# Kernel tuning notes

Measured on AMD Instinct MI355X. Metric: run time of the kernel, lower is better.

The kernel has to match this reference:

```python
import jax, jax.numpy as jnp
import numpy as np

BN_EPS = 1e-5


def setup_inputs() -> dict:
    key = jax.random.key(0)
    ks = jax.random.split(key, 5)
    B, N, M, C = 2, 8192, 8192, 3
    return {
        "x": jax.random.normal(ks[0], (B, N, C), dtype=jnp.float32),
        "y": jax.random.normal(ks[1], (B, M, C), dtype=jnp.float32),
        "W1": jax.random.normal(ks[2], (256, 20), dtype=jnp.float32) * 0.1,
        "gamma1": jnp.ones((256,), jnp.float32),
        "beta1": jnp.zeros((256,), jnp.float32),
        "mean1": jnp.zeros((256,), jnp.float32),
        "var1": jnp.ones((256,), jnp.float32),
        "W2": jax.random.normal(ks[3], (128, 256), dtype=jnp.float32) * 0.1,
        "gamma2": jnp.ones((128,), jnp.float32),
        "beta2": jnp.zeros((128,), jnp.float32),
        "mean2": jnp.zeros((128,), jnp.float32),
        "var2": jnp.ones((128,), jnp.float32),
        "W3": jax.random.normal(ks[4], (1, 128), dtype=jnp.float32) * 0.1,
        "k": 20,
    }


def _bn(x, gamma, beta, mean, var):
    # x: [B, C, N]; inference-mode BatchNorm1d
    inv = gamma * jax.lax.rsqrt(var + BN_EPS)
    return x * inv[None, :, None] + (beta - mean * inv)[None, :, None]


def reference(x, y, W1, gamma1, beta1, mean1, var1,
              W2, gamma2, beta2, mean2, var2, W3, k):
    # x: [B,N,C], y: [B,M,C]
    xx = jnp.sum(x * x, axis=-1)                      # [B,N]
    yy = jnp.sum(y * y, axis=-1)                      # [B,M]
    inner = jnp.einsum('bnc,bmc->bnm', x, y)          # [B,N,M]
    # negative squared pairwise distance (as in torch code)
    pd = 2.0 * inner - xx[:, :, None] - yy[:, None, :]
    dist, _ = jax.lax.top_k(pd, k)                    # [B,N,k], descending = k nearest
    feat = jnp.transpose(dist, (0, 2, 1))             # [B,k,N]
    h = jax.nn.relu(_bn(jnp.einsum('oc,bcn->bon', W1, feat), gamma1, beta1, mean1, var1))
    h = jax.nn.relu(_bn(jnp.einsum('oc,bcn->bon', W2, h), gamma2, beta2, mean2, var2))
    out = jax.nn.sigmoid(jnp.einsum('oc,bcn->bon', W3, h))  # [B,1,N]
    return jnp.transpose(out, (0, 2, 1))              # [B,N,1]
```

## Files before the change

### kernel.cpp

```cpp
#include <hip/hip_runtime.h>
#include <hip/hip_bf16.h>
#include <math.h>


#define M_CAND 8192
#define NROWS 16384
#define KSEL 20
#define MPL 4

__device__ __forceinline__ float med3f(float a, float b, float c) {
    return __builtin_amdgcn_fmed3f(a, b, c);
}

__global__ __launch_bounds__(256) void k_prep(const float* __restrict__ y,
                                              const float* __restrict__ w2,
                                              float* __restrict__ ys,
                                              float* __restrict__ w2t) {
    int idx = blockIdx.x * 256 + threadIdx.x;
    if (idx < NROWS) {
        int b = idx >> 13, m = idx & 8191;
        const float* p = y + (size_t)idx * 3;
        float y0 = p[0], y1 = p[1], y2 = p[2];
        float* base = ys + (size_t)b * 4 * M_CAND + m;
        base[0]          = y0;
        base[M_CAND]     = y1;
        base[2 * M_CAND] = y2;
        base[3 * M_CAND] = -(y0 * y0 + y1 * y1 + y2 * y2);
    } else {
        int j = idx - NROWS;
        int o = j >> 8, kk = j & 255;
        w2t[kk * 128 + o] = w2[j];
    }
}

__global__ __launch_bounds__(256, 4) void k_knn(const float* __restrict__ x,
                                                const float* __restrict__ ys,
                                                float* __restrict__ dfeat) {
    __shared__ float sm[4][64 * 21];
    const int wid  = threadIdx.x >> 6;
    const int lane = threadIdx.x & 63;
    const int row  = blockIdx.x * 4 + wid;
    const int b    = row >> 13;
    const float x0 = x[row * 3 + 0];
    const float x1 = x[row * 3 + 1];
    const float x2 = x[row * 3 + 2];
    const float tx0 = 2.0f * x0, tx1 = 2.0f * x1, tx2 = 2.0f * x2;
    const float xxn = -(x0 * x0 + x1 * x1 + x2 * x2);
    const float4* q0 = (const float4*)(ys + (size_t)(b * 4 + 0) * M_CAND) + lane;
    const float4* q1 = (const float4*)(ys + (size_t)(b * 4 + 1) * M_CAND) + lane;
    const float4* q2 = (const float4*)(ys + (size_t)(b * 4 + 2) * M_CAND) + lane;
    const float4* q3 = (const float4*)(ys + (size_t)(b * 4 + 3) * M_CAND) + lane;

    float bl[MPL];
#pragma unroll
    for (int j = 0; j < MPL; ++j) bl[j] = -3.0e38f;

    float4 c0 = q0[0], c1 = q1[0], c2 = q2[0], c3 = q3[0];
#pragma unroll 1
    for (int t = 0; t < 32; ++t) {
        const int nt = ((t + 1) & 31) * 64;
        float4 n0 = q0[nt], n1 = q1[nt], n2 = q2[nt], n3 = q3[nt];
        const float* e0 = (const float*)&c0;
        const float* e1 = (const float*)&c1;
        const float* e2 = (const float*)&c2;
        const float* e3 = (const float*)&c3;
#pragma unroll
        for (int j = 0; j < 4; ++j) {
            float v = fmaf(tx0, e0[j], fmaf(tx1, e1[j], fmaf(tx2, e2[j], xxn))) + e3[j];
            bl[3] = med3f(v, bl[2], bl[3]);
            bl[2] = med3f(v, bl[1], bl[2]);
            bl[1] = med3f(v, bl[0], bl[1]);
            bl[0] = fmaxf(bl[0], v);
        }
        c0 = n0; c1 = n1; c2 = n2; c3 = n3;
    }

    float* myp = sm[wid] + lane * (MPL + 1);
#pragma unroll
    for (int j = 0; j < MPL; ++j) myp[j] = bl[j];
    myp[MPL] = -3.0e38f;
    asm volatile("s_waitcnt lgkmcnt(0)" ::: "memory");

    int ptr = 0;
    float sel = 0.0f;
    for (int r = 0; r < KSEL; ++r) {
        float head = myp[ptr];
        float mx = head;
#pragma unroll
        for (int off = 32; off >= 1; off >>= 1) mx = fmaxf(mx, __shfl_xor(mx, off, 64));
        unsigned long long ball = __ballot(head == mx);
        int winner = (int)__ffsll(ball) - 1;
        ptr += (lane == winner) ? 1 : 0;
        if (lane == r) sel = mx;
    }

    bool need_exact = (__ballot(ptr >= MPL) != 0ULL);
    if (need_exact) {
        float a[KSEL];
#pragma unroll
        for (int j = 0; j < KSEL; ++j) a[j] = -3.0e38f;
        for (int t = 0; t < 32; ++t) {
            float4 d0 = q0[t * 64], d1 = q1[t * 64], d2 = q2[t * 64], d3 = q3[t * 64];
            const float* e0 = (const float*)&d0;
            const float* e1 = (const float*)&d1;
            const float* e2 = (const float*)&d2;
            const float* e3 = (const float*)&d3;
#pragma unroll
            for (int j = 0; j < 4; ++j) {
                float v = fmaf(tx0, e0[j], fmaf(tx1, e1[j], fmaf(tx2, e2[j], xxn))) + e3[j];
#pragma unroll
                for (int jj = KSEL - 1; jj >= 1; --jj) a[jj] = med3f(v, a[jj - 1], a[jj]);
                a[0] = fmaxf(a[0], v);
            }
        }
        float* mq = sm[wid] + lane * (KSEL + 1);
#pragma unroll
        for (int j = 0; j < KSEL; ++j) mq[j] = a[j];
        mq[KSEL] = -3.0e38f;
        asm volatile("s_waitcnt lgkmcnt(0)" ::: "memory");
        int ptr2 = 0;
        for (int r = 0; r < KSEL; ++r) {
            float head = mq[ptr2];
            float mx = head;
#pragma unroll
            for (int off = 32; off >= 1; off >>= 1) mx = fmaxf(mx, __shfl_xor(mx, off, 64));
            unsigned long long ball = __ballot(head == mx);
            int winner = (int)__ffsll(ball) - 1;
            ptr2 += (lane == winner) ? 1 : 0;
            if (lane == r) sel = mx;
        }
    }

    if (lane < KSEL) dfeat[row * KSEL + lane] = sel;
}

__global__ __launch_bounds__(256) void k_mlp(const float* __restrict__ dfeat,
                                             const float* __restrict__ W1,
                                             const float* __restrict__ g1,
                                             const float* __restrict__ be1,
                                             const float* __restrict__ mu1,
                                             const float* __restrict__ va1,
                                             const float* __restrict__ W2T,
                                             const float* __restrict__ g2,
                                             const float* __restrict__ be2,
                                             const float* __restrict__ mu2,
                                             const float* __restrict__ va2,
                                             const float* __restrict__ W3,
                                             float* __restrict__ out) {
    __shared__ float h1l[32 * 260];
    __shared__ float w2l[256 * 64];
    __shared__ float featl[640];
    const int t = threadIdx.x;
    const int rowbase = blockIdx.x * 32;

    for (int i = t; i < 160; i += 256)
        ((float4*)featl)[i] = *(const float4*)(dfeat + (size_t)rowbase * KSEL + i * 4);
    {
        const int oo4 = (t & 15) * 4;
        const int k0  = t >> 4;
        for (int i = 0; i < 16; ++i) {
            int k = k0 + 16 * i;
            *(float4*)(&w2l[k * 64 + oo4]) = *(const float4*)(W2T + k * 128 + oo4);
        }
    }

    float w[KSEL];
#pragma unroll
    for (int j = 0; j < KSEL; j += 4) {
        float4 q = *(const float4*)(W1 + t * KSEL + j);
        w[j] = q.x; w[j + 1] = q.y; w[j + 2] = q.z; w[j + 3] = q.w;
    }
    const float s1  = g1[t] * rsqrtf(va1[t] + 1e-5f);
    const float bc1 = be1[t] - mu1[t] * s1;

    __syncthreads();

    for (int r = 0; r < 32; ++r) {
        const float* fr = featl + r * KSEL;
        float acc0 = 0.f, acc1 = 0.f;
#pragma unroll
        for (int j = 0; j < KSEL; j += 2) {
            acc0 = fmaf(w[j], fr[j], acc0);
            acc1 = fmaf(w[j + 1], fr[j + 1], acc1);
        }
        h1l[r * 260 + t] = fmaxf(0.f, fmaf(s1, acc0 + acc1, bc1));
    }
    __syncthreads();

    const int og = t & 15;
    const int rq = t >> 4;
    float cacc[2] = {0.f, 0.f};

    for (int half = 0; half < 2; ++half) {
        if (half == 1) {
            __syncthreads();
            const int oo4 = (t & 15) * 4;
            const int k0  = t >> 4;
            for (int i = 0; i < 16; ++i) {
                int k = k0 + 16 * i;
                *(float4*)(&w2l[k * 64 + oo4]) = *(const float4*)(W2T + k * 128 + 64 + oo4);
            }
            __syncthreads();
        }

        float acc[2][4];
#pragma unroll
        for (int r = 0; r < 2; ++r)
#pragma unroll
            for (int i = 0; i < 4; ++i) acc[r][i] = 0.f;

        for (int kq = 0; kq < 64; ++kq) {
            const int k = kq * 4;
            float4 hq[2];
#pragma unroll
            for (int rr = 0; rr < 2; ++rr)
                hq[rr] = *(const float4*)(&h1l[(rq * 2 + rr) * 260 + k]);
            float4 wq[4];
#pragma unroll
            for (int kk = 0; kk < 4; ++kk)
                wq[kk] = *(const float4*)(&w2l[(k + kk) * 64 + og * 4]);
#pragma unroll
            for (int r = 0; r < 2; ++r) {
                const float* hh = (const float*)&hq[r];
#pragma unroll
                for (int kk = 0; kk < 4; ++kk) {
                    const float* ww = (const float*)&wq[kk];
                    const float hval = hh[kk];
#pragma unroll
                    for (int i = 0; i < 4; ++i)
                        acc[r][i] = fmaf(hval, ww[i], acc[r][i]);
                }
            }
        }

        float s2v[4], b2v[4], w3v[4];
#pragma unroll
        for (int i = 0; i < 4; ++i) {
            const int o = half * 64 + og * 4 + i;
            const float sv = g2[o] * rsqrtf(va2[o] + 1e-5f);
            s2v[i] = sv;
            b2v[i] = be2[o] - mu2[o] * sv;
            w3v[i] = W3[o];
        }
#pragma unroll
        for (int r = 0; r < 2; ++r) {
            float c = 0.f;
#pragma unroll
            for (int i = 0; i < 4; ++i) {
                float h2 = fmaxf(0.f, fmaf(s2v[i], acc[r][i], b2v[i]));
                c = fmaf(w3v[i], h2, c);
            }
#pragma unroll
            for (int off = 8; off >= 1; off >>= 1) c += __shfl_xor(c, off, 64);
            cacc[r] += c;
        }
    }

    if (og == 0) {
#pragma unroll
        for (int r = 0; r < 2; ++r) {
            float z = cacc[r];
            out[rowbase + rq * 2 + r] = 1.0f / (1.0f + expf(-z));
        }
    }
}

extern "C" void kernel_launch(void* const* d_in, const int* in_sizes, int n_in,
                              void* d_out, int out_size, void* d_ws, size_t ws_size,
                              hipStream_t stream) {
    const float* x   = (const float*)d_in[0];
    const float* y   = (const float*)d_in[1];
    const float* W1  = (const float*)d_in[2];
    const float* g1  = (const float*)d_in[3];
    const float* be1 = (const float*)d_in[4];
    const float* mu1 = (const float*)d_in[5];
    const float* va1 = (const float*)d_in[6];
    const float* W2  = (const float*)d_in[7];
    const float* g2  = (const float*)d_in[8];
    const float* be2 = (const float*)d_in[9];
    const float* mu2 = (const float*)d_in[10];
    const float* va2 = (const float*)d_in[11];
    const float* W3  = (const float*)d_in[12];
    float* out = (float*)d_out;

    char* ws = (char*)d_ws;
    float* ys    = (float*)(ws);
    float* dfeat = (float*)(ws + 262144);
    float* w2t   = (float*)(ws + 262144 + 1310720);

    k_prep<<<192, 256, 0, stream>>>(y, W2, ys, w2t);
    k_knn <<<4096, 256, 0, stream>>>(x, ys, dfeat);
    k_mlp <<<512, 256, 0, stream>>>(dfeat, W1, g1, be1, mu1, va1,
                                    w2t, g2, be2, mu2, va2, W3, out);
}
```

Measured before the change: 127.6 us.

## Process four query rows per wave with packed-pair candidate layout and streamlined MLP

The kNN kernel now has each wave handle four query rows, so every candidate load is reused across four rows. Candidates are repacked into interleaved float4 pairs so packed two-wide FMAs can compute two distances at once, and the grid shrinks to 1024 blocks. The MLP kernel drops its LDS staging of W2 and features, reading them directly from global memory and computing all 128 outputs in one pass. The trade-off is more registers per thread in kNN and more global and L1 traffic for W2 in the MLP.

```diff
diff --git a/kernel.cpp b/kernel.cpp
--- a/kernel.cpp
+++ b/kernel.cpp
@@ -7,131 +7,182 @@
 #define NROWS 16384
 #define KSEL 20
 #define MPL 4
+#define RPW 4
+
+typedef float v2f __attribute__((ext_vector_type(2)));
 
 __device__ __forceinline__ float med3f(float a, float b, float c) {
     return __builtin_amdgcn_fmed3f(a, b, c);
 }
 
+__device__ __forceinline__ v2f fma2(v2f a, v2f b, v2f c) {
+#if __has_builtin(__builtin_elementwise_fma)
+    return __builtin_elementwise_fma(a, b, c);
+#else
+    v2f r; r.x = fmaf(a.x, b.x, c.x); r.y = fmaf(a.y, b.y, c.y); return r;
+#endif
+}
+
 __global__ __launch_bounds__(256) void k_prep(const float* __restrict__ y,
                                               const float* __restrict__ w2,
-                                              float* __restrict__ ys,
+                                              float4* __restrict__ ysp,
                                               float* __restrict__ w2t) {
     int idx = blockIdx.x * 256 + threadIdx.x;
-    if (idx < NROWS) {
-        int b = idx >> 13, m = idx & 8191;
-        const float* p = y + (size_t)idx * 3;
-        float y0 = p[0], y1 = p[1], y2 = p[2];
-        float* base = ys + (size_t)b * 4 * M_CAND + m;
-        base[0]          = y0;
-        base[M_CAND]     = y1;
-        base[2 * M_CAND] = y2;
-        base[3 * M_CAND] = -(y0 * y0 + y1 * y1 + y2 * y2);
+    if (idx < 8192) {
+        int b = idx >> 12, q = idx & 4095;
+        const float* p0 = y + (size_t)(b * M_CAND + 2 * q) * 3;
+        float a0 = p0[0], a1 = p0[1], a2 = p0[2];
+        float b0 = p0[3], b1 = p0[4], b2 = p0[5];
+        float nwa = -(a0 * a0 + a1 * a1 + a2 * a2);
+        float nwb = -(b0 * b0 + b1 * b1 + b2 * b2);
+        float4* base = ysp + b * 8192;
+        base[q]        = make_float4(a0, b0, a1, b1);
+        base[4096 + q] = make_float4(a2, b2, nwa, nwb);
     } else {
-        int j = idx - NROWS;
+        int j = idx - 8192;
         int o = j >> 8, kk = j & 255;
         w2t[kk * 128 + o] = w2[j];
     }
 }
 
 __global__ __launch_bounds__(256, 4) void k_knn(const float* __restrict__ x,
-                                                const float* __restrict__ ys,
+                                                const float4* __restrict__ ysp,
                                                 float* __restrict__ dfeat) {
     __shared__ float sm[4][64 * 21];
     const int wid  = threadIdx.x >> 6;
     const int lane = threadIdx.x & 63;
-    const int row  = blockIdx.x * 4 + wid;
-    const int b    = row >> 13;
-    const float x0 = x[row * 3 + 0];
-    const float x1 = x[row * 3 + 1];
-    const float x2 = x[row * 3 + 2];
-    const float tx0 = 2.0f * x0, tx1 = 2.0f * x1, tx2 = 2.0f * x2;
-    const float xxn = -(x0 * x0 + x1 * x1 + x2 * x2);
-    const float4* q0 = (const float4*)(ys + (size_t)(b * 4 + 0) * M_CAND) + lane;
-    const float4* q1 = (const float4*)(ys + (size_t)(b * 4 + 1) * M_CAND) + lane;
-    const float4* q2 = (const float4*)(ys + (size_t)(b * 4 + 2) * M_CAND) + lane;
-    const float4* q3 = (const float4*)(ys + (size_t)(b * 4 + 3) * M_CAND) + lane;
-
-    float bl[MPL];
-#pragma unroll
-    for (int j = 0; j < MPL; ++j) bl[j] = -3.0e38f;
-
-    float4 c0 = q0[0], c1 = q1[0], c2 = q2[0], c3 = q3[0];
+    const int qbase = (blockIdx.x * 4 + wid) * RPW;
+    const int b = qbase >> 13;
+
+    float tx0[RPW], tx1[RPW], tx2[RPW], xxn[RPW];
+#pragma unroll
+    for (int r = 0; r < RPW; ++r) {
+        float a0 = x[(qbase + r) * 3 + 0];
+        float a1 = x[(qbase + r) * 3 + 1];
+        float a2 = x[(qbase + r) * 3 + 2];
+        tx0[r] = 2.0f * a0; tx1[r] = 2.0f * a1; tx2[r] = 2.0f * a2;
+        xxn[r] = -(a0 * a0 + a1 * a1 + a2 * a2);
+    }
+    const float4* pa = ysp + b * 8192 + lane;
+    const float4* pb = pa + 4096;
+
+    float bl[RPW][MPL];
+#pragma unroll
+    for (int r = 0; r < RPW; ++r)
+#pragma unroll
+        for (int j = 0; j < MPL; ++j) bl[r][j] = -3.0e38f;
+
+#define PROCESS_PAIR(Aq, Bq)                                                   \
+    {                                                                          \
+        v2f y0p = {(Aq).x, (Aq).y};                                            \
+        v2f y1p = {(Aq).z, (Aq).w};                                            \
+        v2f y2p = {(Bq).x, (Bq).y};                                            \
+        v2f nwp = {(Bq).z, (Bq).w};                                            \
+        _Pragma("unroll")                                                      \
+        for (int r = 0; r < RPW; ++r) {                                        \
+            v2f t0 = {tx0[r], tx0[r]};                                         \
+            v2f t1 = {tx1[r], tx1[r]};                                         \
+            v2f t2 = {tx2[r], tx2[r]};                                         \
+            v2f xp = {xxn[r], xxn[r]};                                         \
+            v2f pd = fma2(t0, y0p, fma2(t1, y1p, fma2(t2, y2p, xp))) + nwp;    \
+            float va = pd.x, vb = pd.y;                                        \
+            bl[r][3] = med3f(va, bl[r][2], bl[r][3]);                          \
+            bl[r][2] = med3f(va, bl[r][1], bl[r][2]);                          \
+            bl[r][1] = med3f(va, bl[r][0], bl[r][1]);                          \
+            bl[r][0] = fmaxf(bl[r][0], va);                                    \
+            bl[r][3] = med3f(vb, bl[r][2], bl[r][3]);                          \
+            bl[r][2] = med3f(vb, bl[r][1], bl[r][2]);                          \
+            bl[r][1] = med3f(vb, bl[r][0], bl[r][1]);                          \
+            bl[r][0] = fmaxf(bl[r][0], vb);                                    \
+        }                                                                      \
+    }
+
+    float4 A0 = pa[0], A1 = pa[64], B0 = pb[0], B1 = pb[64];
 #pragma unroll 1
     for (int t = 0; t < 32; ++t) {
-        const int nt = ((t + 1) & 31) * 64;
-        float4 n0 = q0[nt], n1 = q1[nt], n2 = q2[nt], n3 = q3[nt];
-        const float* e0 = (const float*)&c0;
-        const float* e1 = (const float*)&c1;
-        const float* e2 = (const float*)&c2;
-        const float* e3 = (const float*)&c3;
-#pragma unroll
-        for (int j = 0; j < 4; ++j) {
-            float v = fmaf(tx0, e0[j], fmaf(tx1, e1[j], fmaf(tx2, e2[j], xxn))) + e3[j];
-            bl[3] = med3f(v, bl[2], bl[3]);
-            bl[2] = med3f(v, bl[1], bl[2]);
-            bl[1] = med3f(v, bl[0], bl[1]);
-            bl[0] = fmaxf(bl[0], v);
-        }
-        c0 = n0; c1 = n1; c2 = n2; c3 = n3;
+        const int nt = ((t + 1) & 31) * 128;
+        float4 nA0 = pa[nt], nA1 = pa[nt + 64];
+        float4 nB0 = pb[nt], nB1 = pb[nt + 64];
+        PROCESS_PAIR(A0, B0)
+        PROCESS_PAIR(A1, B1)
+        A0 = nA0; A1 = nA1; B0 = nB0; B1 = nB1;
     }
 
     float* myp = sm[wid] + lane * (MPL + 1);
-#pragma unroll
-    for (int j = 0; j < MPL; ++j) myp[j] = bl[j];
-    myp[MPL] = -3.0e38f;
-    asm volatile("s_waitcnt lgkmcnt(0)" ::: "memory");
-
-    int ptr = 0;
-    float sel = 0.0f;
-    for (int r = 0; r < KSEL; ++r) {
-        float head = myp[ptr];
-        float mx = head;
-#pragma unroll
-        for (int off = 32; off >= 1; off >>= 1) mx = fmaxf(mx, __shfl_xor(mx, off, 64));
-        unsigned long long ball = __ballot(head == mx);
-        int winner = (int)__ffsll(ball) - 1;
-        ptr += (lane == winner) ? 1 : 0;
-        if (lane == r) sel = mx;
-    }
-
-    bool need_exact = (__ballot(ptr >= MPL) != 0ULL);
-    if (need_exact) {
-        float a[KSEL];
-#pragma unroll
-        for (int j = 0; j < KSEL; ++j) a[j] = -3.0e38f;
-        for (int t = 0; t < 32; ++t) {
-            float4 d0 = q0[t * 64], d1 = q1[t * 64], d2 = q2[t * 64], d3 = q3[t * 64];
-            const float* e0 = (const float*)&d0;
-            const float* e1 = (const float*)&d1;
-            const float* e2 = (const float*)&d2;
-            const float* e3 = (const float*)&d3;
-#pragma unroll
-            for (int j = 0; j < 4; ++j) {
-                float v = fmaf(tx0, e0[j], fmaf(tx1, e1[j], fmaf(tx2, e2[j], xxn))) + e3[j];
-#pragma unroll
-                for (int jj = KSEL - 1; jj >= 1; --jj) a[jj] = med3f(v, a[jj - 1], a[jj]);
-                a[0] = fmaxf(a[0], v);
-            }
-        }
-        float* mq = sm[wid] + lane * (KSEL + 1);
-#pragma unroll
-        for (int j = 0; j < KSEL; ++j) mq[j] = a[j];
-        mq[KSEL] = -3.0e38f;
+    unsigned needmask = 0;
+#pragma unroll
+    for (int q = 0; q < RPW; ++q) {
+#pragma unroll
+        for (int j = 0; j < MPL; ++j) myp[j] = bl[q][j];
+        myp[MPL] = -3.0e38f;
         asm volatile("s_waitcnt lgkmcnt(0)" ::: "memory");
-        int ptr2 = 0;
+        int ptr = 0;
+        float sel = 0.0f;
         for (int r = 0; r < KSEL; ++r) {
-            float head = mq[ptr2];
+            float head = myp[ptr];
             float mx = head;
 #pragma unroll
             for (int off = 32; off >= 1; off >>= 1) mx = fmaxf(mx, __shfl_xor(mx, off, 64));
             unsigned long long ball = __ballot(head == mx);
             int winner = (int)__ffsll(ball) - 1;
-            ptr2 += (lane == winner) ? 1 : 0;
+            ptr += (lane == winner) ? 1 : 0;
             if (lane == r) sel = mx;
         }
-    }
-
-    if (lane < KSEL) dfeat[row * KSEL + lane] = sel;
+        if (__ballot(ptr >= MPL) != 0ULL) needmask |= (1u << q);
+        if (lane < KSEL) dfeat[(size_t)(qbase + q) * KSEL + lane] = sel;
+    }
+
+    if (needmask != 0) {
+#pragma unroll
+        for (int q = 0; q < RPW; ++q) {
+            if (!(needmask & (1u << q))) continue;
+            float a[KSEL];
+#pragma unroll
+            for (int j = 0; j < KSEL; ++j) a[j] = -3.0e38f;
+#pragma unroll 1
+            for (int t = 0; t < 32; ++t) {
+                float4 dA0 = pa[t * 128], dA1 = pa[t * 128 + 64];
+                float4 dB0 = pb[t * 128], dB1 = pb[t * 128 + 64];
+                v2f t0 = {tx0[q], tx0[q]};
+                v2f t1 = {tx1[q], tx1[q]};
+                v2f t2 = {tx2[q], tx2[q]};
+                v2f xp = {xxn[q], xxn[q]};
+                v2f pd0 = fma2(t0, (v2f){dA0.x, dA0.y},
+                          fma2(t1, (v2f){dA0.z, dA0.w},
+                          fma2(t2, (v2f){dB0.x, dB0.y}, xp))) + (v2f){dB0.z, dB0.w};
+                v2f pd1 = fma2(t0, (v2f){dA1.x, dA1.y},
+                          fma2(t1, (v2f){dA1.z, dA1.w},
+                          fma2(t2, (v2f){dB1.x, dB1.y}, xp))) + (v2f){dB1.z, dB1.w};
+                float vv[4] = {pd0.x, pd0.y, pd1.x, pd1.y};
+#pragma unroll
+                for (int i = 0; i < 4; ++i) {
+                    float v = vv[i];
+#pragma unroll
+                    for (int jj = KSEL - 1; jj >= 1; --jj) a[jj] = med3f(v, a[jj - 1], a[jj]);
+                    a[0] = fmaxf(a[0], v);
+                }
+            }
+            float* mq = sm[wid] + lane * (KSEL + 1);
+#pragma unroll
+            for (int j = 0; j < KSEL; ++j) mq[j] = a[j];
+            mq[KSEL] = -3.0e38f;
+            asm volatile("s_waitcnt lgkmcnt(0)" ::: "memory");
+            int ptr2 = 0;
+            float sel2 = 0.0f;
+            for (int r = 0; r < KSEL; ++r) {
+                float head = mq[ptr2];
+                float mx = head;
+#pragma unroll
+                for (int off = 32; off >= 1; off >>= 1) mx = fmaxf(mx, __shfl_xor(mx, off, 64));
+                unsigned long long ball = __ballot(head == mx);
+                int winner = (int)__ffsll(ball) - 1;
+                ptr2 += (lane == winner) ? 1 : 0;
+                if (lane == r) sel2 = mx;
+            }
+            if (lane < KSEL) dfeat[(size_t)(qbase + q) * KSEL + lane] = sel2;
+        }
+    }
+#undef PROCESS_PAIR
 }
 
 __global__ __launch_bounds__(256) void k_mlp(const float* __restrict__ dfeat,
@@ -148,21 +199,8 @@
                                              const float* __restrict__ W3,
                                              float* __restrict__ out) {
     __shared__ float h1l[32 * 260];
-    __shared__ float w2l[256 * 64];
-    __shared__ float featl[640];
     const int t = threadIdx.x;
     const int rowbase = blockIdx.x * 32;
-
-    for (int i = t; i < 160; i += 256)
-        ((float4*)featl)[i] = *(const float4*)(dfeat + (size_t)rowbase * KSEL + i * 4);
-    {
-        const int oo4 = (t & 15) * 4;
-        const int k0  = t >> 4;
-        for (int i = 0; i < 16; ++i) {
-            int k = k0 + 16 * i;
-            *(float4*)(&w2l[k * 64 + oo4]) = *(const float4*)(W2T + k * 128 + oo4);
-        }
-    }
 
     float w[KSEL];
 #pragma unroll
@@ -173,15 +211,19 @@
     const float s1  = g1[t] * rsqrtf(va1[t] + 1e-5f);
     const float bc1 = be1[t] - mu1[t] * s1;
 
-    __syncthreads();
-
     for (int r = 0; r < 32; ++r) {
-        const float* fr = featl + r * KSEL;
+        const float* dr = dfeat + (size_t)(rowbase + r) * KSEL;
+        float dv[KSEL];
+#pragma unroll
+        for (int j = 0; j < KSEL; j += 4) {
+            float4 q = *(const float4*)(dr + j);
+            dv[j] = q.x; dv[j + 1] = q.y; dv[j + 2] = q.z; dv[j + 3] = q.w;
+        }
         float acc0 = 0.f, acc1 = 0.f;
 #pragma unroll
         for (int j = 0; j < KSEL; j += 2) {
-            acc0 = fmaf(w[j], fr[j], acc0);
-            acc1 = fmaf(w[j + 1], fr[j + 1], acc1);
+            acc0 = fmaf(w[j], dv[j], acc0);
+            acc1 = fmaf(w[j + 1], dv[j + 1], acc1);
         }
         h1l[r * 260 + t] = fmaxf(0.f, fmaf(s1, acc0 + acc1, bc1));
     }
@@ -189,77 +231,64 @@
 
     const int og = t & 15;
     const int rq = t >> 4;
-    float cacc[2] = {0.f, 0.f};
-
-    for (int half = 0; half < 2; ++half) {
-        if (half == 1) {
-            __syncthreads();
-            const int oo4 = (t & 15) * 4;
-            const int k0  = t >> 4;
-            for (int i = 0; i < 16; ++i) {
-                int k = k0 + 16 * i;
-                *(float4*)(&w2l[k * 64 + oo4]) = *(const float4*)(W2T + k * 128 + 64 + oo4);
-            }
-            __syncthreads();
-        }
-
-        float acc[2][4];
-#pragma unroll
-        for (int r = 0; r < 2; ++r)
-#pragma unroll
-            for (int i = 0; i < 4; ++i) acc[r][i] = 0.f;
-
-        for (int kq = 0; kq < 64; ++kq) {
-            const int k = kq * 4;
-            float4 hq[2];
-#pragma unroll
-            for (int rr = 0; rr < 2; ++rr)
-                hq[rr] = *(const float4*)(&h1l[(rq * 2 + rr) * 260 + k]);
-            float4 wq[4];
-#pragma unroll
-            for (int kk = 0; kk < 4; ++kk)
-                wq[kk] = *(const float4*)(&w2l[(k + kk) * 64 + og * 4]);
-#pragma unroll
-            for (int r = 0; r < 2; ++r) {
-                const float* hh = (const float*)&hq[r];
-#pragma unroll
-                for (int kk = 0; kk < 4; ++kk) {
-                    const float* ww = (const float*)&wq[kk];
-                    const float hval = hh[kk];
-#pragma unroll
-                    for (int i = 0; i < 4; ++i)
-                        acc[r][i] = fmaf(hval, ww[i], acc[r][i]);
+    float acc[2][8];
+#pragma unroll
+    for (int r = 0; r < 2; ++r)
+#pragma unroll
+        for (int i = 0; i < 8; ++i) acc[r][i] = 0.f;
+
+    for (int kq = 0; kq < 64; ++kq) {
+        const int k = kq * 4;
+        float4 hq[2];
+#pragma unroll
+        for (int rr = 0; rr < 2; ++rr)
+            hq[rr] = *(const float4*)(&h1l[(rq * 2 + rr) * 260 + k]);
+        float4 wq[8];
+#pragma unroll
+        for (int kk = 0; kk < 4; ++kk) {
+            wq[kk]     = *(const float4*)(W2T + (k + kk) * 128 + og * 4);
+            wq[4 + kk] = *(const float4*)(W2T + (k + kk) * 128 + 64 + og * 4);
+        }
+#pragma unroll
+        for (int r = 0; r < 2; ++r) {
+            const float* hh = (const float*)&hq[r];
+#pragma unroll
+            for (int kk = 0; kk < 4; ++kk) {
+                const float hval = hh[kk];
+                const float* w0 = (const float*)&wq[kk];
+                const float* w1 = (const float*)&wq[4 + kk];
+#pragma unroll
+                for (int i = 0; i < 4; ++i) {
+                    acc[r][i]     = fmaf(hval, w0[i], acc[r][i]);
+                    acc[r][4 + i] = fmaf(hval, w1[i], acc[r][4 + i]);
                 }
             }
         }
-
-        float s2v[4], b2v[4], w3v[4];
+    }
+
+    float s2v[8], b2v[8], w3v[8];
+#pragma unroll
+    for (int h = 0; h < 2; ++h)
 #pragma unroll
         for (int i = 0; i < 4; ++i) {
-            const int o = half * 64 + og * 4 + i;
+            const int o = h * 64 + og * 4 + i;
             const float sv = g2[o] * rsqrtf(va2[o] + 1e-5f);
-            s2v[i] = sv;
-            b2v[i] = be2[o] - mu2[o] * sv;
-            w3v[i] = W3[o];
-        }
-#pragma unroll
-        for (int r = 0; r < 2; ++r) {
-            float c = 0.f;
-#pragma unroll
-            for (int i = 0; i < 4; ++i) {
-                float h2 = fmaxf(0.f, fmaf(s2v[i], acc[r][i], b2v[i]));
-                c = fmaf(w3v[i], h2, c);
-            }
-#pragma unroll
-            for (int off = 8; off >= 1; off >>= 1) c += __shfl_xor(c, off, 64);
-            cacc[r] += c;
-        }
-    }
-
-    if (og == 0) {
-#pragma unroll
-        for (int r = 0; r < 2; ++r) {
-            float z = cacc[r];
+            s2v[h * 4 + i] = sv;
+            b2v[h * 4 + i] = be2[o] - mu2[o] * sv;
+            w3v[h * 4 + i] = W3[o];
+        }
+#pragma unroll
+    for (int r = 0; r < 2; ++r) {
+        float c = 0.f;
+#pragma unroll
+        for (int i = 0; i < 8; ++i) {
+            float h2 = fmaxf(0.f, fmaf(s2v[i], acc[r][i], b2v[i]));
+            c = fmaf(w3v[i], h2, c);
+        }
+#pragma unroll
+        for (int off = 8; off >= 1; off >>= 1) c += __shfl_xor(c, off, 64);
+        if (og == 0) {
+            float z = c;
             out[rowbase + rq * 2 + r] = 1.0f / (1.0f + expf(-z));
         }
     }
@@ -284,12 +313,12 @@
     float* out = (float*)d_out;
 
     char* ws = (char*)d_ws;
-    float* ys    = (float*)(ws);
+    float4* ysp  = (float4*)(ws);
     float* dfeat = (float*)(ws + 262144);
     float* w2t   = (float*)(ws + 262144 + 1310720);
 
-    k_prep<<<192, 256, 0, stream>>>(y, W2, ys, w2t);
-    k_knn <<<4096, 256, 0, stream>>>(x, ys, dfeat);
+    k_prep<<<160, 256, 0, stream>>>(y, W2, ysp, w2t);
+    k_knn <<<1024, 256, 0, stream>>>(x, ysp, dfeat);
     k_mlp <<<512, 256, 0, stream>>>(dfeat, W1, g1, be1, mu1, va1,
                                     w2t, g2, be2, mu2, va2, W3, out);
 }
```

New measurement: 128.1 us. Within noise of the previous version (+0.4%).
